# Kernel tuning notes

Measured on AMD Instinct MI355X. Metric: run time of the kernel, lower is better.

## Reference

```python
import jax, jax.numpy as jnp
import numpy as np

TAU = 0.03        # self.tau
EPS = 0.65       # args.epsilon
EPS2 = 0.4       # args.epsilon2 (trimap)
LOGIT_T = 0.07    # logits temperature


def _l2norm(x, axis):
    # torch F.normalize: x / max(||x||, 1e-12)
    n = jnp.sqrt(jnp.sum(x * x, axis=axis, keepdims=True))
    return x / jnp.maximum(n, 1e-12)


def setup_inputs() -> dict:
    key = jax.random.key(0)
    k1, k2 = jax.random.split(key)
    img = jax.random.normal(k1, (256, 512, 14, 14), dtype=jnp.float32)
    aud = jax.random.normal(k2, (256, 512), dtype=jnp.float32)
    return {"img": img, "aud": aud}


def reference(img, aud):
    # img: [B, C, H, W] backbone vision features; aud: [B, C] pooled audio features
    B = img.shape[0]
    img = _l2norm(img, axis=1)
    aud = _l2norm(aud, axis=1)

    # A: paired audio-visual correlation map [B, 1, H, W]
    A = jnp.einsum('nchw,nc->nhw', img, aud)[:, None]
    # A0: full cross-pair correlation maps [B, B, H, W] (n = image idx, m = audio idx)
    A0 = jnp.einsum('nchw,mc->nmhw', img, aud)
    # AdaptiveMaxPool2d((1,1)) -> max over spatial dims -> [B, B]
    A0_ref = jnp.max(A0, axis=(2, 3))

    Pos = jax.nn.sigmoid((A - EPS) / TAU)           # [B, 1, H, W]
    Pos2 = jax.nn.sigmoid((A - EPS2) / TAU)         # trimap branch
    Neg = 1.0 - Pos2
    Pos_all = jax.nn.sigmoid((A0 - EPS) / TAU)      # [B, B, H, W]

    mask = 1.0 - 100.0 * jnp.eye(B, dtype=img.dtype)
    # gated weighted-mean pooling over spatial dims
    sim = (Pos_all * A0).sum(axis=(2, 3)) / Pos_all.sum(axis=(2, 3)) * mask   # [B, B]
    sim1 = (Pos * A).sum(axis=(2, 3)) / Pos.sum(axis=(2, 3))                  # [B, 1]
    sim2 = (Neg * A).sum(axis=(2, 3)) / Neg.sum(axis=(2, 3))                  # [B, 1]

    logits = jnp.concatenate((sim1, sim, sim2), axis=1) / LOGIT_T             # [B, B+2]
    return (A, logits, Pos, Neg, A0_ref)
```

## Files before the change

### kernel.cpp

```cpp
#include <hip/hip_runtime.h>
#include <math.h>

typedef _Float16 half8 __attribute__((ext_vector_type(8)));
typedef float f32x4 __attribute__((ext_vector_type(4)));

#define RLT (1.0f/0.07f)


__device__ __forceinline__ void gll16(const void* g, void* l) {
    __builtin_amdgcn_global_load_lds(
        (const __attribute__((address_space(1))) void*)g,
        (__attribute__((address_space(3))) void*)l, 16, 0, 0);
}

__global__ __launch_bounds__(256) void prep_aud_pk(const float* __restrict__ aud,
                                                   _Float16* __restrict__ aud_pk) {
    int m = blockIdx.x, t = threadIdx.x;
    float a0 = aud[m * 512 + t];
    float a1 = aud[m * 512 + 256 + t];
    float s = a0 * a0 + a1 * a1;
    #pragma unroll
    for (int off = 32; off; off >>= 1) s += __shfl_down(s, off, 64);
    __shared__ float wsum[4];
    __shared__ float rns;
    if ((t & 63) == 0) wsum[t >> 6] = s;
    __syncthreads();
    if (t == 0) rns = 1.0f / fmaxf(sqrtf(wsum[0] + wsum[1] + wsum[2] + wsum[3]), 1e-12f);
    __syncthreads();
    float rn = rns;
    int c0 = t, c1 = t + 256;
    aud_pk[(c0 >> 3) * 2048 + m * 8 + (c0 & 7)] = (_Float16)(a0 * rn);
    aud_pk[(c1 >> 3) * 2048 + m * 8 + (c1 & 7)] = (_Float16)(a1 * rn);
}

__global__ __launch_bounds__(512, 4) void av_split(const float* __restrict__ img,
                                                   const _Float16* __restrict__ aud_pk,
                                                   float* __restrict__ out,
                                                   float* __restrict__ pmax,
                                                   float* __restrict__ psw,
                                                   float* __restrict__ pswa,
                                                   float* __restrict__ pdiag) {
    const int bid = blockIdx.x;
    const int n = bid >> 1, half = bid & 1;
    const int tid = threadIdx.x;
    const int w = tid >> 6, l = tid & 63;
    const int q = w & 3;
    const int hg = w >> 2;
    const int HT = hg ? 3 : 4;

    __shared__ _Float16 __align__(16) Abuf[2][4][112][8];
    __shared__ _Float16 __align__(16) Bbuf[2][4][256][8];
    __shared__ float nrm_parts[4][98];
    __shared__ float rnorm_s[112];
    __shared__ float red_max[2][256], red_sw[2][256], red_swa[2][256];
    __shared__ float diag_parts[2][4][4];

    if (tid < 112) {
        int b = tid / 56, rem = tid % 56, kg = rem / 14, row = 98 + rem % 14;
        *(float4*)&Abuf[b][kg][row][0] = make_float4(0.f, 0.f, 0.f, 0.f);
    }

    const float* imgn = img + (size_t)n * (512 * 196);
    const bool act = tid < 392;
    const int p   = act ? tid / 98 : 0;
    const int hwl = act ? tid % 98 : 0;
    const int g   = half * 98 + hwl;
    float nrm = 0.f;
    float av[8];

    #define STAGE_B(t, buf)                                                         \
        do {                                                                        \
            const _Float16* g0 = aud_pk + (((size_t)(t) * 1024 + tid) << 3);        \
            _Float16* l0 = &Bbuf[buf][0][0][0] + ((w * 64) << 3);                   \
            gll16(g0, l0);                                                          \
            gll16(g0 + 4096, l0 + 4096);                                            \
        } while (0)

    #define LOAD_A(t)                                                               \
        do {                                                                        \
            if (act) {                                                              \
                const float* src = imgn + ((size_t)(32 * (t) + p * 8)) * 196 + g;   \
                _Pragma("unroll")                                                   \
                for (int i = 0; i < 8; i++) av[i] = src[i * 196];                   \
            }                                                                       \
        } while (0)

    #define STAGE_A(buf)                                                            \
        do {                                                                        \
            if (act) {                                                              \
                half8 h0;                                                           \
                _Pragma("unroll")                                                   \
                for (int i = 0; i < 8; i++) {                                       \
                    h0[i] = (_Float16)av[i];                                        \
                    nrm += av[i] * av[i];                                           \
                }                                                                   \
                *(half8*)&Abuf[buf][p][hwl][0] = h0;                                \
            }                                                                       \
        } while (0)

    STAGE_B(0, 0);
    LOAD_A(0);
    STAGE_A(0);
    __syncthreads();

    f32x4 acc[4][4];
    #pragma unroll
    for (int ht = 0; ht < 4; ht++)
        #pragma unroll
        for (int mt = 0; mt < 4; mt++)
            acc[ht][mt] = (f32x4){0.f, 0.f, 0.f, 0.f};

    const int aoff = (l >> 4) * 896  + (hg * 64 + (l & 15)) * 8;
    const int boff = (l >> 4) * 2048 + (q * 64 + (l & 15)) * 8;

    for (int t = 0; t < 16; t++) {
        const int cur = t & 1, nb = cur ^ 1;
        const bool more = t < 15;
        if (more) {
            STAGE_B(t + 1, nb);
            LOAD_A(t + 1);
        }
        {
            const _Float16* Ab = &Abuf[cur][0][0][0];
            const _Float16* Bb = &Bbuf[cur][0][0][0];
            half8 bfrag[4];
            #pragma unroll
            for (int mt = 0; mt < 4; mt++) bfrag[mt] = *(const half8*)(Bb + boff + mt * 128);
            half8 afrag[4];
            #pragma unroll
            for (int ht = 0; ht < 4; ht++)
                if (ht < HT) afrag[ht] = *(const half8*)(Ab + aoff + ht * 128);
            #pragma unroll
            for (int ht = 0; ht < 4; ht++)
                if (ht < HT)
                    #pragma unroll
                    for (int mt = 0; mt < 4; mt++)
                        acc[ht][mt] = __builtin_amdgcn_mfma_f32_16x16x32_f16(
                            afrag[ht], bfrag[mt], acc[ht][mt], 0, 0, 0);
        }
        if (more) STAGE_A(nb);
        __syncthreads();
    }

    if (act) nrm_parts[p][hwl] = nrm;
    __syncthreads();
    if (tid < 112) {
        float v = 0.f;
        if (tid < 98)
            v = 1.0f / fmaxf(sqrtf(nrm_parts[0][tid] + nrm_parts[1][tid] +
                                   nrm_parts[2][tid] + nrm_parts[3][tid]), 1e-12f);
        rnorm_s[tid] = v;
    }
    __syncthreads();

    float mx[4], sw[4], swa[4];
    #pragma unroll
    for (int mt = 0; mt < 4; mt++) { mx[mt] = -1e30f; sw[mt] = 0.f; swa[mt] = 0.f; }
    float s1n = 0.f, s1d = 0.f, s2n = 0.f, s2d = 0.f;
    const int dmt = (n >> 4) & 3, dq = n >> 6, dl = n & 15;
    const bool isdiag = (q == dq) && ((l & 15) == dl);

    #pragma unroll
    for (int ht = 0; ht < 4; ht++) {
        if (ht < HT) {
            int rowb = hg * 64 + ht * 16 + ((l >> 4) << 2);
            #pragma unroll
            for (int r = 0; r < 4; r++) {
                int row = rowb + r;
                float rn = rnorm_s[row];
                bool valid = row < 98;
                int hw = half * 98 + row;
                #pragma unroll
                for (int mt = 0; mt < 4; mt++) {
                    float a0 = acc[ht][mt][r] * rn;
                    if (valid) {
                        float wg = 1.0f / (1.0f + __expf((0.65f - a0) * (1.0f / 0.03f)));
                        mx[mt]  = fmaxf(mx[mt], a0);
                        sw[mt] += wg;
                        swa[mt] += wg * a0;
                        if (isdiag && mt == dmt) {
                            out[n * 196 + hw] = a0;
                            out[116224 + n * 196 + hw] = wg;
                            float p2 = 1.0f / (1.0f + __expf((0.40f - a0) * (1.0f / 0.03f)));
                            float ng = 1.0f - p2;
                            out[166400 + n * 196 + hw] = ng;
                            s1n += wg * a0; s1d += wg;
                            s2n += ng * a0; s2d += ng;
                        }
                    }
                }
            }
        }
    }

    #pragma unroll
    for (int mt = 0; mt < 4; mt++) {
        float m1 = mx[mt], v1 = sw[mt], v2 = swa[mt];
        m1 = fmaxf(m1, __shfl_xor(m1, 16, 64)); v1 += __shfl_xor(v1, 16, 64); v2 += __shfl_xor(v2, 16, 64);
        m1 = fmaxf(m1, __shfl_xor(m1, 32, 64)); v1 += __shfl_xor(v1, 32, 64); v2 += __shfl_xor(v2, 32, 64);
        if (l < 16) {
            int m = q * 64 + mt * 16 + l;
            red_max[hg][m] = m1; red_sw[hg][m] = v1; red_swa[hg][m] = v2;
        }
    }
    if (isdiag) {
        diag_parts[hg][l >> 4][0] = s1n;
        diag_parts[hg][l >> 4][1] = s1d;
        diag_parts[hg][l >> 4][2] = s2n;
        diag_parts[hg][l >> 4][3] = s2d;
    }
    __syncthreads();

    if (tid < 256) {
        int m = tid;
        int base = (n * 2 + half) * 256 + m;
        pmax[base] = fmaxf(red_max[0][m], red_max[1][m]);
        psw[base]  = red_sw[0][m] + red_sw[1][m];
        pswa[base] = red_swa[0][m] + red_swa[1][m];
    }
    if (tid < 4) {
        float s = 0.f;
        #pragma unroll
        for (int h2 = 0; h2 < 2; h2++)
            #pragma unroll
            for (int lg = 0; lg < 4; lg++)
                s += diag_parts[h2][lg][tid];
        pdiag[(n * 2 + half) * 4 + tid] = s;
    }
    #undef STAGE_B
    #undef LOAD_A
    #undef STAGE_A
}

__global__ __launch_bounds__(256) void av_final(const float* __restrict__ pmax,
                                                const float* __restrict__ psw,
                                                const float* __restrict__ pswa,
                                                const float* __restrict__ pdiag,
                                                float* __restrict__ out) {
    int n = blockIdx.x, m = threadIdx.x;
    int b0 = (n * 2) * 256 + m, b1 = (n * 2 + 1) * 256 + m;
    float mx = fmaxf(pmax[b0], pmax[b1]);
    float sim = (pswa[b0] + pswa[b1]) / (psw[b0] + psw[b1]);
    if (m == n) sim *= -99.0f;
    out[50176 + n * 258 + 1 + m] = sim * RLT;
    out[216576 + n * 256 + m] = mx;
    if (m == n) {
        const float* d = pdiag + n * 8;
        out[50176 + n * 258]       = ((d[0] + d[4]) / (d[1] + d[5])) * RLT;
        out[50176 + n * 258 + 257] = ((d[2] + d[6]) / (d[3] + d[7])) * RLT;
    }
}

extern "C" void kernel_launch(void* const* d_in, const int* in_sizes, int n_in,
                              void* d_out, int out_size, void* d_ws, size_t ws_size,
                              hipStream_t stream) {
    const float* img = (const float*)d_in[0];
    const float* aud = (const float*)d_in[1];
    float* out = (float*)d_out;

    _Float16* aud_pk = (_Float16*)d_ws;
    float* wsf   = (float*)d_ws;
    float* pmax  = wsf + 32768;
    float* psw   = pmax + 131072;
    float* pswa  = psw + 131072;
    float* pdiag = pswa + 131072;

    prep_aud_pk<<<256, 256, 0, stream>>>(aud, aud_pk);
    av_split<<<512, 512, 0, stream>>>(img, aud_pk, out, pmax, psw, pswa, pdiag);
    av_final<<<256, 256, 0, stream>>>(pmax, psw, pswa, pdiag, out);
}
```

Baseline: 42.78 us.

## Load audio B fragments directly from global into registers instead of LDS

Removes the LDS staging buffer for the packed audio operand. Each lane now loads its half8 B fragments straight from global (L2-resident) memory into double-buffered registers, and the loop is unrolled by two to alternate the register buffers. This frees 32KB of LDS and cuts LDS traffic per step. The cost is redundant global loads across waves and more register pressure. The workspace offset for the partial buffers also moves.

```diff
diff --git a/kernel.cpp b/kernel.cpp
--- a/kernel.cpp
+++ b/kernel.cpp
@@ -6,12 +6,6 @@
 
 #define RLT (1.0f/0.07f)
 
-
-__device__ __forceinline__ void gll16(const void* g, void* l) {
-    __builtin_amdgcn_global_load_lds(
-        (const __attribute__((address_space(1))) void*)g,
-        (__attribute__((address_space(3))) void*)l, 16, 0, 0);
-}
 
 __global__ __launch_bounds__(256) void prep_aud_pk(const float* __restrict__ aud,
                                                    _Float16* __restrict__ aud_pk) {
@@ -33,13 +27,13 @@
     aud_pk[(c1 >> 3) * 2048 + m * 8 + (c1 & 7)] = (_Float16)(a1 * rn);
 }
 
-__global__ __launch_bounds__(512, 4) void av_split(const float* __restrict__ img,
-                                                   const _Float16* __restrict__ aud_pk,
-                                                   float* __restrict__ out,
-                                                   float* __restrict__ pmax,
-                                                   float* __restrict__ psw,
-                                                   float* __restrict__ pswa,
-                                                   float* __restrict__ pdiag) {
+__global__ __launch_bounds__(512, 4) void av_split2(const float* __restrict__ img,
+                                                    const _Float16* __restrict__ aud_pk,
+                                                    float* __restrict__ out,
+                                                    float* __restrict__ pmax,
+                                                    float* __restrict__ psw,
+                                                    float* __restrict__ pswa,
+                                                    float* __restrict__ pdiag) {
     const int bid = blockIdx.x;
     const int n = bid >> 1, half = bid & 1;
     const int tid = threadIdx.x;
@@ -49,7 +43,6 @@
     const int HT = hg ? 3 : 4;
 
     __shared__ _Float16 __align__(16) Abuf[2][4][112][8];
-    __shared__ _Float16 __align__(16) Bbuf[2][4][256][8];
     __shared__ float nrm_parts[4][98];
     __shared__ float rnorm_s[112];
     __shared__ float red_max[2][256], red_sw[2][256], red_swa[2][256];
@@ -68,12 +61,14 @@
     float nrm = 0.f;
     float av[8];
 
-    #define STAGE_B(t, buf)                                                         \
-        do {                                                                        \
-            const _Float16* g0 = aud_pk + (((size_t)(t) * 1024 + tid) << 3);        \
-            _Float16* l0 = &Bbuf[buf][0][0][0] + ((w * 64) << 3);                   \
-            gll16(g0, l0);                                                          \
-            gll16(g0 + 4096, l0 + 4096);                                            \
+    const int kk = l >> 4, lm = l & 15;
+    const _Float16* bbase = aud_pk + ((size_t)(kk * 256 + q * 64 + lm) << 3);
+
+    #define LOAD_B(dst, t)                                                          \
+        do {                                                                        \
+            _Pragma("unroll")                                                       \
+            for (int mt = 0; mt < 4; mt++)                                          \
+                dst[mt] = *(const half8*)(bbase + (size_t)(t) * 8192 + mt * 128);   \
         } while (0)
 
     #define LOAD_A(t)                                                               \
@@ -98,9 +93,10 @@
             }                                                                       \
         } while (0)
 
-    STAGE_B(0, 0);
     LOAD_A(0);
     STAGE_A(0);
+    half8 b0[4], b1[4];
+    LOAD_B(b0, 0);
     __syncthreads();
 
     f32x4 acc[4][4];
@@ -110,36 +106,32 @@
         for (int mt = 0; mt < 4; mt++)
             acc[ht][mt] = (f32x4){0.f, 0.f, 0.f, 0.f};
 
-    const int aoff = (l >> 4) * 896  + (hg * 64 + (l & 15)) * 8;
-    const int boff = (l >> 4) * 2048 + (q * 64 + (l & 15)) * 8;
-
-    for (int t = 0; t < 16; t++) {
-        const int cur = t & 1, nb = cur ^ 1;
-        const bool more = t < 15;
-        if (more) {
-            STAGE_B(t + 1, nb);
-            LOAD_A(t + 1);
-        }
-        {
-            const _Float16* Ab = &Abuf[cur][0][0][0];
-            const _Float16* Bb = &Bbuf[cur][0][0][0];
-            half8 bfrag[4];
-            #pragma unroll
-            for (int mt = 0; mt < 4; mt++) bfrag[mt] = *(const half8*)(Bb + boff + mt * 128);
-            half8 afrag[4];
-            #pragma unroll
-            for (int ht = 0; ht < 4; ht++)
-                if (ht < HT) afrag[ht] = *(const half8*)(Ab + aoff + ht * 128);
-            #pragma unroll
-            for (int ht = 0; ht < 4; ht++)
-                if (ht < HT)
-                    #pragma unroll
-                    for (int mt = 0; mt < 4; mt++)
-                        acc[ht][mt] = __builtin_amdgcn_mfma_f32_16x16x32_f16(
-                            afrag[ht], bfrag[mt], acc[ht][mt], 0, 0, 0);
-        }
-        if (more) STAGE_A(nb);
-        __syncthreads();
+    const int aoff = kk * 896 + (hg * 64 + lm) * 8;
+
+    #define STEP(t, cur, bcur, bnxt, more)                                          \
+        do {                                                                        \
+            if (more) { LOAD_A((t) + 1); LOAD_B(bnxt, (t) + 1); }                   \
+            {                                                                       \
+                const _Float16* Ab = &Abuf[cur][0][0][0];                           \
+                half8 afrag[4];                                                     \
+                _Pragma("unroll")                                                   \
+                for (int ht = 0; ht < 4; ht++)                                      \
+                    if (ht < HT) afrag[ht] = *(const half8*)(Ab + aoff + ht * 128); \
+                _Pragma("unroll")                                                   \
+                for (int ht = 0; ht < 4; ht++)                                      \
+                    if (ht < HT)                                                    \
+                        _Pragma("unroll")                                           \
+                        for (int mt = 0; mt < 4; mt++)                              \
+                            acc[ht][mt] = __builtin_amdgcn_mfma_f32_16x16x32_f16(   \
+                                afrag[ht], bcur[mt], acc[ht][mt], 0, 0, 0);         \
+            }                                                                       \
+            if (more) STAGE_A((cur) ^ 1);                                           \
+            __syncthreads();                                                        \
+        } while (0)
+
+    for (int tt = 0; tt < 16; tt += 2) {
+        STEP(tt,     0, b0, b1, true);
+        STEP(tt + 1, 1, b1, b0, (tt + 1) < 15);
     }
 
     if (act) nrm_parts[p][hwl] = nrm;
@@ -158,12 +150,12 @@
     for (int mt = 0; mt < 4; mt++) { mx[mt] = -1e30f; sw[mt] = 0.f; swa[mt] = 0.f; }
     float s1n = 0.f, s1d = 0.f, s2n = 0.f, s2d = 0.f;
     const int dmt = (n >> 4) & 3, dq = n >> 6, dl = n & 15;
-    const bool isdiag = (q == dq) && ((l & 15) == dl);
+    const bool isdiag = (q == dq) && (lm == dl);
 
     #pragma unroll
     for (int ht = 0; ht < 4; ht++) {
         if (ht < HT) {
-            int rowb = hg * 64 + ht * 16 + ((l >> 4) << 2);
+            int rowb = hg * 64 + ht * 16 + (kk << 2);
             #pragma unroll
             for (int r = 0; r < 4; r++) {
                 int row = rowb + r;
@@ -204,10 +196,10 @@
         }
     }
     if (isdiag) {
-        diag_parts[hg][l >> 4][0] = s1n;
-        diag_parts[hg][l >> 4][1] = s1d;
-        diag_parts[hg][l >> 4][2] = s2n;
-        diag_parts[hg][l >> 4][3] = s2d;
+        diag_parts[hg][kk][0] = s1n;
+        diag_parts[hg][kk][1] = s1d;
+        diag_parts[hg][kk][2] = s2n;
+        diag_parts[hg][kk][3] = s2d;
     }
     __syncthreads();
 
@@ -227,7 +219,8 @@
                 s += diag_parts[h2][lg][tid];
         pdiag[(n * 2 + half) * 4 + tid] = s;
     }
-    #undef STAGE_B
+    #undef STEP
+    #undef LOAD_B
     #undef LOAD_A
     #undef STAGE_A
 }
@@ -260,12 +253,12 @@
 
     _Float16* aud_pk = (_Float16*)d_ws;
     float* wsf   = (float*)d_ws;
-    float* pmax  = wsf + 32768;
+    float* pmax  = wsf + 65536;
     float* psw   = pmax + 131072;
     float* pswa  = psw + 131072;
     float* pdiag = pswa + 131072;
 
     prep_aud_pk<<<256, 256, 0, stream>>>(aud, aud_pk);
-    av_split<<<512, 512, 0, stream>>>(img, aud_pk, out, pmax, psw, pswa, pdiag);
+    av_split2<<<512, 512, 0, stream>>>(img, aud_pk, out, pmax, psw, pswa, pdiag);
     av_final<<<256, 256, 0, stream>>>(pmax, psw, pswa, pdiag, out);
 }
```

Measured after the change: 71.46 us. 67.0% more time.
